# Kernel tuning notes

Hardware: AMD Instinct MI355X
Metric: run time of the kernel (lower is better)

The kernel has to match this reference:

```python
import jax, jax.numpy as jnp
import numpy as np
from jax import lax

N_HEAD, D_IN, D_HID, D_OUT = 8, 64, 64, 64
SEQ = 32768
STD = 1.0 / np.sqrt(D_HID * N_HEAD)


def _unif(key, shape):
    return jax.random.uniform(key, shape, jnp.float32, -STD, STD)


def setup_inputs() -> dict:
    key = jax.random.key(0)
    ks = jax.random.split(key, 12)
    D = N_HEAD * D_IN
    return {
        "inputs": jax.random.normal(ks[0], (SEQ, D), jnp.float32),
        "W_in": _unif(ks[1], (D, D)),
        "b_in": _unif(ks[2], (D,)),
        "W_gates": _unif(ks[3], (D_IN, 3 * D_HID)),
        "b_gates": _unif(ks[4], (3 * D_HID,)),
        "W_og": _unif(ks[5], (D_IN, D_HID)),
        "b_og": _unif(ks[6], (D_HID,)),
        "W_c": _unif(ks[7], (D_HID, D_OUT)),
        "b_c": _unif(ks[8], (D_OUT,)),
        "W_out": _unif(ks[9], (N_HEAD * D_OUT, N_HEAD * D_OUT)),
        "b_out": _unif(ks[10], (N_HEAD * D_OUT,)),
    }


def reference(inputs, W_in, b_in, W_gates, b_gates, W_og, b_og, W_c, b_c, W_out, b_out):
    S = inputs.shape[0]
    # input mixing across heads, then flatten: (S, H*d_in) -> (S*H, d_in)
    x = (inputs @ W_in + b_in).reshape(S * N_HEAD, D_IN)
    # FirstModule: fused gate projection
    g = x @ W_gates + b_gates  # (S*H, 3*d_hid)
    fg = jax.nn.sigmoid(g[:, :D_HID])
    ig = jax.nn.sigmoid(g[:, D_HID:2 * D_HID])
    h = jnp.tanh(g[:, 2 * D_HID:])
    hr = ig * h
    # linear recurrence c_t = fg_t * c_{t-1} + hr_t, c_0 = 0, via associative scan
    def comb(e1, e2):
        a1, b1 = e1
        a2, b2 = e2
        return (a1 * a2, b1 * a2 + b2)
    _, c = lax.associative_scan(comb, (fg, hr))  # (S*H, d_hid)
    # SecondModule: output gate and projection
    og = jax.nn.sigmoid(x @ W_og + b_og)
    o = (og * c) @ W_c + b_c  # (S*H, d_out)
    o = o.reshape(S, N_HEAD * D_OUT)
    return o @ W_out + b_out
```

## Files before the change

### kernel.cpp

```cpp
#include <hip/hip_runtime.h>


typedef unsigned short ushort;
typedef __bf16 bf16x8 __attribute__((ext_vector_type(8)));
typedef float f32x4 __attribute__((ext_vector_type(4)));

#define CROWS 64
#define NCH  4096
#define NSUP 64

#define GLOAD16(gp, lp) __builtin_amdgcn_global_load_lds( \
    (const __attribute__((address_space(1))) void*)(gp),  \
    (__attribute__((address_space(3))) void*)(lp), 16, 0, 0)

__device__ inline float b2f(ushort u) {
    return __builtin_bit_cast(float, (unsigned)u << 16);
}
__device__ inline ushort f2b(float f) {
    unsigned x = __builtin_bit_cast(unsigned, f);
    x += 0x7FFFu + ((x >> 16) & 1u);
    return (ushort)(x >> 16);
}
__device__ inline float sigm(float v) { return __builtin_amdgcn_rcpf(1.0f + __expf(-v)); }
__device__ inline float tanh_fast(float v) {
    return 2.0f * __builtin_amdgcn_rcpf(1.0f + __expf(-2.0f * v)) - 1.0f;
}
__device__ inline f32x4 MFMA(bf16x8 a, bf16x8 b, f32x4 c) {
    return __builtin_amdgcn_mfma_f32_16x16x32_bf16(a, b, c, 0, 0, 0);
}

__global__ void transpose512(const float* __restrict__ src, ushort* __restrict__ dst) {
    __shared__ float tile[32][33];
    const int tx = threadIdx.x & 31, ty = threadIdx.x >> 5;
    const int x0 = blockIdx.x * 32, y0 = blockIdx.y * 32;
    #pragma unroll
    for (int dy = 0; dy < 32; dy += 8)
        tile[ty + dy][tx] = src[(size_t)(y0 + ty + dy) * 512 + x0 + tx];
    __syncthreads();
    #pragma unroll
    for (int dy = 0; dy < 32; dy += 8)
        dst[(size_t)(x0 + ty + dy) * 512 + y0 + tx] = f2b(tile[tx][ty + dy]);
}

__global__ void prep_small(const float* __restrict__ W_gates, const float* __restrict__ W_og,
                           const float* __restrict__ W_c,
                           const float* __restrict__ b_gates, const float* __restrict__ b_og,
                           ushort* __restrict__ W2T, ushort* __restrict__ WcT, float* __restrict__ b2) {
    const int idx = blockIdx.x * 256 + threadIdx.x;
    if (idx < 16384) {
        const int n = idx >> 6, k = idx & 63;
        float v;
        if      (n < 64)  v = W_gates[k * 192 + 64 + n];
        else if (n < 128) v = W_gates[k * 192 + 128 + (n - 64)];
        else if (n < 192) v = W_gates[k * 192 + (n - 128)];
        else              v = W_og[k * 64 + (n - 192)];
        W2T[idx] = f2b(v);
    } else if (idx < 16384 + 4096) {
        const int i = idx - 16384;
        const int n = i >> 6, k = i & 63;
        WcT[i] = f2b(W_c[(k << 6) + n]);
    } else if (idx < 16384 + 4096 + 256) {
        const int i = idx - 20480;
        float v;
        if      (i < 64)  v = b_gates[64 + i];
        else if (i < 128) v = b_gates[128 + (i - 64)];
        else if (i < 192) v = b_gates[i - 128];
        else              v = b_og[i - 192];
        b2[i] = v;
    }
}

__global__ __launch_bounds__(256)
void cvt_f32_bf16(const float* __restrict__ src, ushort* __restrict__ dst) {
    const long i = ((long)blockIdx.x * 256 + threadIdx.x) * 8;
    const float4 v0 = *(const float4*)(src + i);
    const float4 v1 = *(const float4*)(src + i + 4);
    *(ushort4*)(dst + i)     = make_ushort4(f2b(v0.x), f2b(v0.y), f2b(v0.z), f2b(v0.w));
    *(ushort4*)(dst + i + 4) = make_ushort4(f2b(v1.x), f2b(v1.y), f2b(v1.z), f2b(v1.w));
}

template <int BM, int BN, int WAVES_M, int WAVES_N, int A32, int C32>
__global__ __launch_bounds__(256)
void gemm_bt(const void* __restrict__ Av, const ushort* __restrict__ Bt,
             const float* __restrict__ bias, void* __restrict__ Cv,
             int M, int N, int K) {
    constexpr int WM = BM / WAVES_M, WN = BN / WAVES_N;
    constexpr int MT = WM / 16, NT = WN / 16;
    __shared__ __align__(16) ushort sA[BM * 32];
    __shared__ __align__(16) ushort sB[BN * 32];

    const int t = threadIdx.x, w = t >> 6, lane = t & 63;
    const int wm = (w / WAVES_N) * WM, wn = (w % WAVES_N) * WN;
    const long bm = (long)blockIdx.x * BM, bn = (long)blockIdx.y * BN;

    f32x4 acc[MT][NT] = {};

    for (int k0 = 0; k0 < K; k0 += 32) {
        if (A32) {
            const float* A = (const float*)Av;
            #pragma unroll
            for (int is = 0; is < BM / 32; ++is) {
                const int row = is * 32 + (t >> 3);
                const int cd = (t & 7) >> 1, half = t & 1;
                const float4 v = *(const float4*)(A + (bm + row) * (long)K + k0 + (t & 7) * 4);
                *(ushort4*)&sA[row * 32 + ((cd ^ (row & 3)) * 8) + half * 4] =
                    make_ushort4(f2b(v.x), f2b(v.y), f2b(v.z), f2b(v.w));
            }
        } else {
            const ushort* A = (const ushort*)Av;
            #pragma unroll
            for (int is = 0; is < BM / 64; ++is) {
                const int row = t >> 2, kc = t & 3;
                GLOAD16(A + (bm + is * 64 + row) * (long)K + k0 + ((kc ^ (row & 3)) * 8),
                        (char*)sA + is * 4096 + w * 1024);
            }
        }
        #pragma unroll
        for (int is = 0; is < BN / 64; ++is) {
            const int row = t >> 2, kc = t & 3;
            GLOAD16(Bt + (bn + is * 64 + row) * (long)K + k0 + ((kc ^ (row & 3)) * 8),
                    (char*)sB + is * 4096 + w * 1024);
        }
        __syncthreads();

        bf16x8 af[MT], bfr[NT];
        #pragma unroll
        for (int i = 0; i < MT; ++i) {
            const int row = wm + i * 16 + (lane & 15), c = lane >> 4;
            af[i] = *(const bf16x8*)&sA[row * 32 + ((c ^ (row & 3)) * 8)];
        }
        #pragma unroll
        for (int j = 0; j < NT; ++j) {
            const int rb = wn + j * 16 + (lane & 15), c = lane >> 4;
            bfr[j] = *(const bf16x8*)&sB[rb * 32 + ((c ^ (rb & 3)) * 8)];
        }
        #pragma unroll
        for (int i = 0; i < MT; ++i)
            #pragma unroll
            for (int j = 0; j < NT; ++j)
                acc[i][j] = MFMA(af[i], bfr[j], acc[i][j]);
        __syncthreads();
    }

    #pragma unroll
    for (int i = 0; i < MT; ++i)
        #pragma unroll
        for (int j = 0; j < NT; ++j) {
            const long col = bn + wn + j * 16 + (lane & 15);
            const float bv = bias[col];
            #pragma unroll
            for (int r = 0; r < 4; ++r) {
                const long row = bm + wm + i * 16 + ((lane >> 4) << 2) + r;
                const float v = acc[i][j][r] + bv;
                if (C32) ((float*)Cv)[row * (long)N + col] = v;
                else     ((ushort*)Cv)[row * (long)N + col] = f2b(v);
            }
        }
}

__global__ __launch_bounds__(256, 4)
void gates_store(const ushort* __restrict__ X, const ushort* __restrict__ W2T,
                 const float* __restrict__ b2,
                 unsigned* __restrict__ FGHR, ushort* __restrict__ OGg,
                 float* __restrict__ Agg, float* __restrict__ Bgg) {
    __shared__ __align__(16) char smem[29696];
    ushort* sFG = (ushort*)smem;
    ushort* sHR = (ushort*)(smem + 9216);
    ushort* sOG = (ushort*)(smem + 18432);
    float*  spa = (float*)(smem + 27648);
    float*  spb = (float*)(smem + 28672);

    const int t = threadIdx.x, w = t >> 6, lane = t & 63;
    const int blk = blockIdx.x;
    const long row0 = (long)blk * CROWS;

    const int wm = (w >> 1) * 32;
    const int grpB = w & 1;
    const int colbase = grpB * 128;
    const int lr = lane & 15, lc = lane >> 4;

    bf16x8 af[2][2];
    #pragma unroll
    for (int kk = 0; kk < 2; ++kk)
        #pragma unroll
        for (int i = 0; i < 2; ++i)
            af[kk][i] = *(const bf16x8*)(X + (row0 + wm + i * 16 + lr) * 64 + kk * 32 + lc * 8);

    f32x4 acc[2][8] = {};
    #pragma unroll
    for (int kk = 0; kk < 2; ++kk)
        #pragma unroll
        for (int j = 0; j < 8; ++j) {
            const bf16x8 bf = *(const bf16x8*)(W2T + (colbase + j * 16 + lr) * 64 + kk * 32 + lc * 8);
            acc[0][j] = MFMA(af[kk][0], bf, acc[0][j]);
            acc[1][j] = MFMA(af[kk][1], bf, acc[1][j]);
        }

    if (!grpB) {
        #pragma unroll
        for (int jj = 0; jj < 4; ++jj) {
            const int ch = jj * 16 + lr;
            const float bi = b2[ch], bh = b2[64 + ch];
            #pragma unroll
            for (int i = 0; i < 2; ++i)
                #pragma unroll
                for (int r = 0; r < 4; ++r) {
                    const int row = wm + i * 16 + (lc << 2) + r;
                    const float gi = acc[i][jj][r] + bi;
                    const float gh = acc[i][jj + 4][r] + bh;
                    sHR[row * 72 + ch] = f2b(sigm(gi) * tanh_fast(gh));
                }
        }
    } else {
        #pragma unroll
        for (int jj = 0; jj < 4; ++jj) {
            const int ch = jj * 16 + lr;
            const float bfg = b2[128 + ch], bog = b2[192 + ch];
            #pragma unroll
            for (int i = 0; i < 2; ++i)
                #pragma unroll
                for (int r = 0; r < 4; ++r) {
                    const int row = wm + i * 16 + (lc << 2) + r;
                    sFG[row * 72 + ch] = f2b(sigm(acc[i][jj][r] + bfg));
                    sOG[row * 72 + ch] = f2b(sigm(acc[i][jj + 4][r] + bog));
                }
        }
    }
    __syncthreads();

    {
        const int ch = lane;
        float a = 1.0f, b = 0.0f;
        #pragma unroll
        for (int r = 0; r < 16; ++r) {
            const int row = (w << 4) + r;
            const ushort ufg = sFG[row * 72 + ch];
            const ushort uhr = sHR[row * 72 + ch];
            FGHR[(row0 + row) * 64 + ch] = (unsigned)ufg | ((unsigned)uhr << 16);
            OGg[(row0 + row) * 64 + ch] = sOG[row * 72 + ch];
            const float fg = b2f(ufg), hr = b2f(uhr);
            a *= fg;
            b = fmaf(b, fg, hr);
        }
        spa[(w << 6) + ch] = a;
        spb[(w << 6) + ch] = b;
    }
    __syncthreads();

    if (t < 64) {
        float a = spa[t], b = spb[t];
        #pragma unroll
        for (int k = 1; k < 4; ++k) {
            const float a2 = spa[(k << 6) + t];
            const float bb = spb[(k << 6) + t];
            a *= a2;
            b = fmaf(b, a2, bb);
        }
        Agg[blk * 64 + t] = a;
        Bgg[blk * 64 + t] = b;
    }
}

__global__ __launch_bounds__(256, 4)
void scan_apply(const unsigned* __restrict__ FGHR, const ushort* __restrict__ OGg,
                const float* __restrict__ Agg, const float* __restrict__ Bgg,
                const float* __restrict__ PreS,
                const ushort* __restrict__ WcT, const float* __restrict__ b_c,
                ushort* __restrict__ O) {
    __shared__ __align__(16) char smem[10240];
    ushort* sP  = (ushort*)smem;
    float*  spa = (float*)(smem + 8192);
    float*  spb = (float*)(smem + 9216);

    const int t = threadIdx.x, w = t >> 6, lane = t & 63;
    const int blk = blockIdx.x;
    const long row0 = (long)blk * CROWS;
    const int ch = lane;

    unsigned fh[16];
    {
        float a = 1.0f, b = 0.0f;
        #pragma unroll
        for (int r = 0; r < 16; ++r) {
            fh[r] = FGHR[(row0 + (w << 4) + r) * 64 + ch];
            const float fg = b2f((ushort)fh[r]);
            const float hr = b2f((ushort)(fh[r] >> 16));
            a *= fg;
            b = fmaf(b, fg, hr);
        }
        spa[(w << 6) + ch] = a;
        spb[(w << 6) + ch] = b;
    }
    __syncthreads();

    float c = fmaf(PreS[(blk >> 6) * 64 + ch], Agg[blk * 64 + ch], Bgg[blk * 64 + ch]);
    for (int k = 0; k < w; ++k)
        c = fmaf(c, spa[(k << 6) + ch], spb[(k << 6) + ch]);

    const int cch = ch >> 3, half = ch & 7;
    #pragma unroll
    for (int r = 0; r < 16; ++r) {
        const int row = (w << 4) + r;
        const float fg = b2f((ushort)fh[r]);
        const float hr = b2f((ushort)(fh[r] >> 16));
        c = fmaf(c, fg, hr);
        const float og = b2f(OGg[(row0 + row) * 64 + ch]);
        sP[row * 64 + ((cch ^ (row & 7)) * 8) + half] = f2b(og * c);
    }
    __syncthreads();

    const int wm = (w >> 1) * 32;
    const int wn2 = (w & 1) * 32;
    const int lr = lane & 15, lc = lane >> 4;
    f32x4 acc2[2][2] = {};
    #pragma unroll
    for (int kk = 0; kk < 2; ++kk) {
        bf16x8 pa[2], wb[2];
        #pragma unroll
        for (int i = 0; i < 2; ++i) {
            const int row = wm + i * 16 + lr, cidx = kk * 4 + lc;
            pa[i] = *(const bf16x8*)&sP[row * 64 + ((cidx ^ (row & 7)) * 8)];
        }
        #pragma unroll
        for (int j = 0; j < 2; ++j)
            wb[j] = *(const bf16x8*)(WcT + (wn2 + j * 16 + lr) * 64 + kk * 32 + lc * 8);
        #pragma unroll
        for (int i = 0; i < 2; ++i)
            #pragma unroll
            for (int j = 0; j < 2; ++j)
                acc2[i][j] = MFMA(pa[i], wb[j], acc2[i][j]);
    }
    #pragma unroll
    for (int i = 0; i < 2; ++i)
        #pragma unroll
        for (int j = 0; j < 2; ++j) {
            const int col = wn2 + j * 16 + lr;
            const float bv = b_c[col];
            #pragma unroll
            for (int r = 0; r < 4; ++r) {
                const int row = wm + i * 16 + (lc << 2) + r;
                O[(row0 + row) * 64 + col] = f2b(acc2[i][j][r] + bv);
            }
        }
}

template <int APPLY>
__global__ __launch_bounds__(256, 4)
void gates_scan(const ushort* __restrict__ X, const ushort* __restrict__ W2T,
                const float* __restrict__ b2, const ushort* __restrict__ WcT,
                const float* __restrict__ b_c,
                float* __restrict__ Agg, float* __restrict__ Bgg,
                const float* __restrict__ PreS, ushort* __restrict__ O) {
    __shared__ __align__(16) char smem[APPLY ? 35840 : 18432];
    ushort* sFG = (ushort*)smem;
    ushort* sHR = (ushort*)(smem + 9216);
    ushort* sOG = (ushort*)(smem + 18432);
    ushort* sP  = (ushort*)(smem + 27648);

    const int t = threadIdx.x, w = t >> 6, lane = t & 63;
    const int blk = blockIdx.x;
    const long row0 = (long)blk * CROWS;

    const int wm = (w >> 1) * 32;
    const int grpB = w & 1;
    const int colbase = grpB * 128;
    const int lr = lane & 15, lc = lane >> 4;

    bf16x8 af[2][2];
    #pragma unroll
    for (int kk = 0; kk < 2; ++kk)
        #pragma unroll
        for (int i = 0; i < 2; ++i)
            af[kk][i] = *(const bf16x8*)(X + (row0 + wm + i * 16 + lr) * 64 + kk * 32 + lc * 8);

    f32x4 acc[2][8] = {};
    #pragma unroll
    for (int kk = 0; kk < 2; ++kk)
        #pragma unroll
        for (int j = 0; j < 8; ++j) {
            const bf16x8 bf = *(const bf16x8*)(W2T + (colbase + j * 16 + lr) * 64 + kk * 32 + lc * 8);
            acc[0][j] = MFMA(af[kk][0], bf, acc[0][j]);
            acc[1][j] = MFMA(af[kk][1], bf, acc[1][j]);
        }

    if (!grpB) {
        #pragma unroll
        for (int jj = 0; jj < 4; ++jj) {
            const int ch = jj * 16 + lr;
            const float bi = b2[ch], bh = b2[64 + ch];
            #pragma unroll
            for (int i = 0; i < 2; ++i)
                #pragma unroll
                for (int r = 0; r < 4; ++r) {
                    const int row = wm + i * 16 + (lc << 2) + r;
                    const float gi = acc[i][jj][r] + bi;
                    const float gh = acc[i][jj + 4][r] + bh;
                    sHR[row * 72 + ch] = f2b(sigm(gi) * tanh_fast(gh));
                }
        }
    } else {
        #pragma unroll
        for (int jj = 0; jj < 4; ++jj) {
            const int ch = jj * 16 + lr;
            const float bfg = b2[128 + ch], bog = b2[192 + ch];
            #pragma unroll
            for (int i = 0; i < 2; ++i)
                #pragma unroll
                for (int r = 0; r < 4; ++r) {
                    const int row = wm + i * 16 + (lc << 2) + r;
                    sFG[row * 72 + ch] = f2b(sigm(acc[i][jj][r] + bfg));
                    if (APPLY) sOG[row * 72 + ch] = f2b(sigm(acc[i][jj + 4][r] + bog));
                }
        }
    }
    __syncthreads();

    if (!APPLY) {
        if (t < 64) {
            float a = 1.0f, b = 0.0f;
            #pragma unroll 8
            for (int r = 0; r < CROWS; ++r) {
                const float fg = b2f(sFG[r * 72 + t]);
                const float hr = b2f(sHR[r * 72 + t]);
                a *= fg;
                b = fmaf(b, fg, hr);
            }
            Agg[blk * 64 + t] = a;
            Bgg[blk * 64 + t] = b;
        }
        return;
    }

    if (t < 64) {
        float c = fmaf(PreS[(blk >> 6) * 64 + t], Agg[blk * 64 + t], Bgg[blk * 64 + t]);
        const int cch = t >> 3, half = t & 7;
        #pragma unroll 8
        for (int r = 0; r < CROWS; ++r) {
            const float fg = b2f(sFG[r * 72 + t]);
            const float hr = b2f(sHR[r * 72 + t]);
            c = fmaf(c, fg, hr);
            sP[r * 64 + ((cch ^ (r & 7)) * 8) + half] = f2b(b2f(sOG[r * 72 + t]) * c);
        }
    }
    __syncthreads();

    const int wn2 = grpB * 32;
    f32x4 acc2[2][2] = {};
    #pragma unroll
    for (int kk = 0; kk < 2; ++kk) {
        bf16x8 pa[2], wb[2];
        #pragma unroll
        for (int i = 0; i < 2; ++i) {
            const int row = wm + i * 16 + lr, c = kk * 4 + lc;
            pa[i] = *(const bf16x8*)&sP[row * 64 + ((c ^ (row & 7)) * 8)];
        }
        #pragma unroll
        for (int j = 0; j < 2; ++j)
            wb[j] = *(const bf16x8*)(WcT + (wn2 + j * 16 + lr) * 64 + kk * 32 + lc * 8);
        #pragma unroll
        for (int i = 0; i < 2; ++i)
            #pragma unroll
            for (int j = 0; j < 2; ++j)
                acc2[i][j] = MFMA(pa[i], wb[j], acc2[i][j]);
    }
    #pragma unroll
    for (int i = 0; i < 2; ++i)
        #pragma unroll
        for (int j = 0; j < 2; ++j) {
            const int col = wn2 + j * 16 + lr;
            const float bv = b_c[col];
            #pragma unroll
            for (int r = 0; r < 4; ++r) {
                const int row = wm + i * 16 + (lc << 2) + r;
                O[(row0 + row) * 64 + col] = f2b(acc2[i][j][r] + bv);
            }
        }
}

__global__ void scan_super(float* __restrict__ Agg, float* __restrict__ Bgg,
                           float* __restrict__ SA, float* __restrict__ SB) {
    const int s = blockIdx.x, ch = threadIdx.x;
    float a = 1.0f, b = 0.0f;
    #pragma unroll 8
    for (int j = 0; j < 64; ++j) {
        const int idx = (s * 64 + j) * 64 + ch;
        const float a2 = Agg[idx], bb = Bgg[idx];
        Agg[idx] = a;
        Bgg[idx] = b;
        a *= a2;
        b = fmaf(b, a2, bb);
    }
    SA[s * 64 + ch] = a;
    SB[s * 64 + ch] = b;
}

__global__ void scan_top(const float* __restrict__ SA, const float* __restrict__ SB,
                         float* __restrict__ PreS) {
    const int ch = threadIdx.x;
    float c = 0.0f;
    #pragma unroll 8
    for (int s = 0; s < 64; ++s) {
        PreS[s * 64 + ch] = c;
        c = fmaf(c, SA[s * 64 + ch], SB[s * 64 + ch]);
    }
}

extern "C" void kernel_launch(void* const* d_in, const int* in_sizes, int n_in,
                              void* d_out, int out_size, void* d_ws, size_t ws_size,
                              hipStream_t stream) {
    const float* inputs  = (const float*)d_in[0];
    const float* W_in    = (const float*)d_in[1];
    const float* b_in    = (const float*)d_in[2];
    const float* W_gates = (const float*)d_in[3];
    const float* b_gates = (const float*)d_in[4];
    const float* W_og    = (const float*)d_in[5];
    const float* b_og    = (const float*)d_in[6];
    const float* W_c     = (const float*)d_in[7];
    const float* b_c     = (const float*)d_in[8];
    const float* W_out   = (const float*)d_in[9];
    const float* b_out   = (const float*)d_in[10];
    float* out = (float*)d_out;

    char* ws = (char*)d_ws;
    ushort* X     = (ushort*)(ws);
    ushort* WinT  = (ushort*)(ws + 33554432);
    ushort* WoutT = (ushort*)(ws + 34078720);
    ushort* W2T   = (ushort*)(ws + 34603008);
    ushort* WcT   = (ushort*)(ws + 34635776);
    float*  b2    = (float*)(ws + 34643968);
    float*  Agg   = (float*)(ws + 34644992);
    float*  Bgg   = (float*)(ws + 35693568);
    float*  SA    = (float*)(ws + 36742144);
    float*  SB    = (float*)(ws + 36758528);
    float*  PreS  = (float*)(ws + 36774912);
    ushort* Ibf   = (ushort*)(ws + 36791296);
    unsigned* FGHR = (unsigned*)(ws + 36791296);
    ushort* OGg   = (ushort*)d_out;
    ushort* O = X;

    const bool new_path = ws_size >= 103900160ull;
    const bool big_ws   = ws_size >= 70345728ull;

    transpose512<<<dim3(16, 16), 256, 0, stream>>>(W_in, WinT);
    transpose512<<<dim3(16, 16), 256, 0, stream>>>(W_out, WoutT);
    prep_small<<<81, 256, 0, stream>>>(W_gates, W_og, W_c, b_gates, b_og, W2T, WcT, b2);

    if (new_path) {
        cvt_f32_bf16<<<8192, 256, 0, stream>>>(inputs, Ibf);
        gemm_bt<128, 128, 2, 2, 0, 0><<<dim3(256, 4), 256, 0, stream>>>(
            Ibf, WinT, b_in, X, 32768, 512, 512);
        gates_store<<<NCH, 256, 0, stream>>>(X, W2T, b2, FGHR, OGg, Agg, Bgg);
        scan_super<<<NSUP, 64, 0, stream>>>(Agg, Bgg, SA, SB);
        scan_top<<<1, 64, 0, stream>>>(SA, SB, PreS);
        scan_apply<<<NCH, 256, 0, stream>>>(FGHR, OGg, Agg, Bgg, PreS, WcT, b_c, O);
    } else if (big_ws) {
        cvt_f32_bf16<<<8192, 256, 0, stream>>>(inputs, Ibf);
        gemm_bt<128, 128, 2, 2, 0, 0><<<dim3(256, 4), 256, 0, stream>>>(
            Ibf, WinT, b_in, X, 32768, 512, 512);
        gates_scan<0><<<NCH, 256, 0, stream>>>(X, W2T, b2, WcT, b_c, Agg, Bgg, PreS, O);
        scan_super<<<NSUP, 64, 0, stream>>>(Agg, Bgg, SA, SB);
        scan_top<<<1, 64, 0, stream>>>(SA, SB, PreS);
        gates_scan<1><<<NCH, 256, 0, stream>>>(X, W2T, b2, WcT, b_c, Agg, Bgg, PreS, O);
    } else {
        gemm_bt<128, 128, 2, 2, 1, 0><<<dim3(256, 4), 256, 0, stream>>>(
            inputs, WinT, b_in, X, 32768, 512, 512);
        gates_scan<0><<<NCH, 256, 0, stream>>>(X, W2T, b2, WcT, b_c, Agg, Bgg, PreS, O);
        scan_super<<<NSUP, 64, 0, stream>>>(Agg, Bgg, SA, SB);
        scan_top<<<1, 64, 0, stream>>>(SA, SB, PreS);
        gates_scan<1><<<NCH, 256, 0, stream>>>(X, W2T, b2, WcT, b_c, Agg, Bgg, PreS, O);
    }

    gemm_bt<128, 128, 2, 2, 0, 1><<<dim3(256, 4), 256, 0, stream>>>(
        O, WoutT, b_out, out, 32768, 512, 512);
}
```

Before: 288.6 us.

## Recompute output gate in scan_apply instead of storing it from gates_store

The output-gate projection and sigmoid move from gates_store into scan_apply, which reloads X and the og slice of W2T and recomputes og with MFMAs into shared memory. This removes a global write and a later read of the bf16 OG tensor, which is the same size as the per-head activation. In exchange, X is read a second time in scan_apply and a few more MFMAs are added there. gates_store uses less LDS and declares a higher launch_bounds occupancy target to fit more blocks per CU.

```diff
diff --git a/kernel.cpp b/kernel.cpp
--- a/kernel.cpp
+++ b/kernel.cpp
@@ -158,17 +158,16 @@
         }
 }
 
-__global__ __launch_bounds__(256, 4)
+__global__ __launch_bounds__(256, 6)
 void gates_store(const ushort* __restrict__ X, const ushort* __restrict__ W2T,
                  const float* __restrict__ b2,
-                 unsigned* __restrict__ FGHR, ushort* __restrict__ OGg,
+                 unsigned* __restrict__ FGHR,
                  float* __restrict__ Agg, float* __restrict__ Bgg) {
-    __shared__ __align__(16) char smem[29696];
+    __shared__ __align__(16) char smem[20480];
     ushort* sFG = (ushort*)smem;
     ushort* sHR = (ushort*)(smem + 9216);
-    ushort* sOG = (ushort*)(smem + 18432);
-    float*  spa = (float*)(smem + 27648);
-    float*  spb = (float*)(smem + 28672);
+    float*  spa = (float*)(smem + 18432);
+    float*  spb = (float*)(smem + 19456);
 
     const int t = threadIdx.x, w = t >> 6, lane = t & 63;
     const int blk = blockIdx.x;
@@ -176,7 +175,6 @@
 
     const int wm = (w >> 1) * 32;
     const int grpB = w & 1;
-    const int colbase = grpB * 128;
     const int lr = lane & 15, lc = lane >> 4;
 
     bf16x8 af[2][2];
@@ -187,14 +185,25 @@
             af[kk][i] = *(const bf16x8*)(X + (row0 + wm + i * 16 + lr) * 64 + kk * 32 + lc * 8);
 
     f32x4 acc[2][8] = {};
-    #pragma unroll
-    for (int kk = 0; kk < 2; ++kk)
-        #pragma unroll
-        for (int j = 0; j < 8; ++j) {
-            const bf16x8 bf = *(const bf16x8*)(W2T + (colbase + j * 16 + lr) * 64 + kk * 32 + lc * 8);
-            acc[0][j] = MFMA(af[kk][0], bf, acc[0][j]);
-            acc[1][j] = MFMA(af[kk][1], bf, acc[1][j]);
-        }
+    if (!grpB) {
+        #pragma unroll
+        for (int kk = 0; kk < 2; ++kk)
+            #pragma unroll
+            for (int j = 0; j < 8; ++j) {
+                const bf16x8 bf = *(const bf16x8*)(W2T + (j * 16 + lr) * 64 + kk * 32 + lc * 8);
+                acc[0][j] = MFMA(af[kk][0], bf, acc[0][j]);
+                acc[1][j] = MFMA(af[kk][1], bf, acc[1][j]);
+            }
+    } else {
+        #pragma unroll
+        for (int kk = 0; kk < 2; ++kk)
+            #pragma unroll
+            for (int j = 0; j < 4; ++j) {
+                const bf16x8 bf = *(const bf16x8*)(W2T + ((128 + j * 16 + lr)) * 64 + kk * 32 + lc * 8);
+                acc[0][j] = MFMA(af[kk][0], bf, acc[0][j]);
+                acc[1][j] = MFMA(af[kk][1], bf, acc[1][j]);
+            }
+    }
 
     if (!grpB) {
         #pragma unroll
@@ -215,14 +224,13 @@
         #pragma unroll
         for (int jj = 0; jj < 4; ++jj) {
             const int ch = jj * 16 + lr;
-            const float bfg = b2[128 + ch], bog = b2[192 + ch];
+            const float bfg = b2[128 + ch];
             #pragma unroll
             for (int i = 0; i < 2; ++i)
                 #pragma unroll
                 for (int r = 0; r < 4; ++r) {
                     const int row = wm + i * 16 + (lc << 2) + r;
                     sFG[row * 72 + ch] = f2b(sigm(acc[i][jj][r] + bfg));
-                    sOG[row * 72 + ch] = f2b(sigm(acc[i][jj + 4][r] + bog));
                 }
         }
     }
@@ -237,7 +245,6 @@
             const ushort ufg = sFG[row * 72 + ch];
             const ushort uhr = sHR[row * 72 + ch];
             FGHR[(row0 + row) * 64 + ch] = (unsigned)ufg | ((unsigned)uhr << 16);
-            OGg[(row0 + row) * 64 + ch] = sOG[row * 72 + ch];
             const float fg = b2f(ufg), hr = b2f(uhr);
             a *= fg;
             b = fmaf(b, fg, hr);
@@ -262,20 +269,36 @@
 }
 
 __global__ __launch_bounds__(256, 4)
-void scan_apply(const unsigned* __restrict__ FGHR, const ushort* __restrict__ OGg,
+void scan_apply(const unsigned* __restrict__ FGHR, const ushort* __restrict__ X,
+                const ushort* __restrict__ W2T, const float* __restrict__ b2,
                 const float* __restrict__ Agg, const float* __restrict__ Bgg,
                 const float* __restrict__ PreS,
                 const ushort* __restrict__ WcT, const float* __restrict__ b_c,
                 ushort* __restrict__ O) {
-    __shared__ __align__(16) char smem[10240];
+    __shared__ __align__(16) char smem[19456];
     ushort* sP  = (ushort*)smem;
-    float*  spa = (float*)(smem + 8192);
-    float*  spb = (float*)(smem + 9216);
+    ushort* sOG = (ushort*)(smem + 8192);
+    float*  spa = (float*)(smem + 17408);
+    float*  spb = (float*)(smem + 18432);
 
     const int t = threadIdx.x, w = t >> 6, lane = t & 63;
     const int blk = blockIdx.x;
     const long row0 = (long)blk * CROWS;
     const int ch = lane;
+    const int lr = lane & 15, lc = lane >> 4;
+    const int wm = (w >> 1) * 32;
+    const int wno = (w & 1) * 32;
+
+    bf16x8 af[2][2], wb[2][2];
+    #pragma unroll
+    for (int kk = 0; kk < 2; ++kk) {
+        #pragma unroll
+        for (int i = 0; i < 2; ++i)
+            af[kk][i] = *(const bf16x8*)(X + (row0 + wm + i * 16 + lr) * 64 + kk * 32 + lc * 8);
+        #pragma unroll
+        for (int j = 0; j < 2; ++j)
+            wb[kk][j] = *(const bf16x8*)(W2T + (192 + wno + j * 16 + lr) * 64 + kk * 32 + lc * 8);
+    }
 
     unsigned fh[16];
     {
@@ -291,6 +314,29 @@
         spa[(w << 6) + ch] = a;
         spb[(w << 6) + ch] = b;
     }
+
+    {
+        f32x4 aog[2][2] = {};
+        #pragma unroll
+        for (int kk = 0; kk < 2; ++kk)
+            #pragma unroll
+            for (int i = 0; i < 2; ++i)
+                #pragma unroll
+                for (int j = 0; j < 2; ++j)
+                    aog[i][j] = MFMA(af[kk][i], wb[kk][j], aog[i][j]);
+        #pragma unroll
+        for (int i = 0; i < 2; ++i)
+            #pragma unroll
+            for (int j = 0; j < 2; ++j) {
+                const int col = wno + j * 16 + lr;
+                const float bog = b2[192 + col];
+                #pragma unroll
+                for (int r = 0; r < 4; ++r) {
+                    const int row = wm + i * 16 + (lc << 2) + r;
+                    sOG[row * 72 + col] = f2b(sigm(aog[i][j][r] + bog));
+                }
+            }
+    }
     __syncthreads();
 
     float c = fmaf(PreS[(blk >> 6) * 64 + ch], Agg[blk * 64 + ch], Bgg[blk * 64 + ch]);
@@ -304,18 +350,15 @@
         const float fg = b2f((ushort)fh[r]);
         const float hr = b2f((ushort)(fh[r] >> 16));
         c = fmaf(c, fg, hr);
-        const float og = b2f(OGg[(row0 + row) * 64 + ch]);
+        const float og = b2f(sOG[row * 72 + ch]);
         sP[row * 64 + ((cch ^ (row & 7)) * 8) + half] = f2b(og * c);
     }
     __syncthreads();
 
-    const int wm = (w >> 1) * 32;
-    const int wn2 = (w & 1) * 32;
-    const int lr = lane & 15, lc = lane >> 4;
     f32x4 acc2[2][2] = {};
     #pragma unroll
     for (int kk = 0; kk < 2; ++kk) {
-        bf16x8 pa[2], wb[2];
+        bf16x8 pa[2], wc[2];
         #pragma unroll
         for (int i = 0; i < 2; ++i) {
             const int row = wm + i * 16 + lr, cidx = kk * 4 + lc;
@@ -323,18 +366,18 @@
         }
         #pragma unroll
         for (int j = 0; j < 2; ++j)
-            wb[j] = *(const bf16x8*)(WcT + (wn2 + j * 16 + lr) * 64 + kk * 32 + lc * 8);
+            wc[j] = *(const bf16x8*)(WcT + (wno + j * 16 + lr) * 64 + kk * 32 + lc * 8);
         #pragma unroll
         for (int i = 0; i < 2; ++i)
             #pragma unroll
             for (int j = 0; j < 2; ++j)
-                acc2[i][j] = MFMA(pa[i], wb[j], acc2[i][j]);
+                acc2[i][j] = MFMA(pa[i], wc[j], acc2[i][j]);
     }
     #pragma unroll
     for (int i = 0; i < 2; ++i)
         #pragma unroll
         for (int j = 0; j < 2; ++j) {
-            const int col = wn2 + j * 16 + lr;
+            const int col = wno + j * 16 + lr;
             const float bv = b_c[col];
             #pragma unroll
             for (int r = 0; r < 4; ++r) {
@@ -448,7 +491,7 @@
     f32x4 acc2[2][2] = {};
     #pragma unroll
     for (int kk = 0; kk < 2; ++kk) {
-        bf16x8 pa[2], wb[2];
+        bf16x8 pa[2], wbx[2];
         #pragma unroll
         for (int i = 0; i < 2; ++i) {
             const int row = wm + i * 16 + lr, c = kk * 4 + lc;
@@ -456,12 +499,12 @@
         }
         #pragma unroll
         for (int j = 0; j < 2; ++j)
-            wb[j] = *(const bf16x8*)(WcT + (wn2 + j * 16 + lr) * 64 + kk * 32 + lc * 8);
+            wbx[j] = *(const bf16x8*)(WcT + (wn2 + j * 16 + lr) * 64 + kk * 32 + lc * 8);
         #pragma unroll
         for (int i = 0; i < 2; ++i)
             #pragma unroll
             for (int j = 0; j < 2; ++j)
-                acc2[i][j] = MFMA(pa[i], wb[j], acc2[i][j]);
+                acc2[i][j] = MFMA(pa[i], wbx[j], acc2[i][j]);
     }
     #pragma unroll
     for (int i = 0; i < 2; ++i)
@@ -535,7 +578,6 @@
     float*  PreS  = (float*)(ws + 36774912);
     ushort* Ibf   = (ushort*)(ws + 36791296);
     unsigned* FGHR = (unsigned*)(ws + 36791296);
-    ushort* OGg   = (ushort*)d_out;
     ushort* O = X;
 
     const bool new_path = ws_size >= 103900160ull;
@@ -549,10 +591,10 @@
         cvt_f32_bf16<<<8192, 256, 0, stream>>>(inputs, Ibf);
         gemm_bt<128, 128, 2, 2, 0, 0><<<dim3(256, 4), 256, 0, stream>>>(
             Ibf, WinT, b_in, X, 32768, 512, 512);
-        gates_store<<<NCH, 256, 0, stream>>>(X, W2T, b2, FGHR, OGg, Agg, Bgg);
+        gates_store<<<NCH, 256, 0, stream>>>(X, W2T, b2, FGHR, Agg, Bgg);
         scan_super<<<NSUP, 64, 0, stream>>>(Agg, Bgg, SA, SB);
         scan_top<<<1, 64, 0, stream>>>(SA, SB, PreS);
-        scan_apply<<<NCH, 256, 0, stream>>>(FGHR, OGg, Agg, Bgg, PreS, WcT, b_c, O);
+        scan_apply<<<NCH, 256, 0, stream>>>(FGHR, X, W2T, b2, Agg, Bgg, PreS, WcT, b_c, O);
     } else if (big_ws) {
         cvt_f32_bf16<<<8192, 256, 0, stream>>>(inputs, Ibf);
         gemm_bt<128, 128, 2, 2, 0, 0><<<dim3(256, 4), 256, 0, stream>>>(
```

Result: slower. 318.8 us (+10.5%).

## Fuse gate, scan and output projection via decoupled look-back scan

Applied to the files above, without the earlier changes.

Replaces the gates_store / scan_super / scan_top / scan_apply chain with one gates_fused kernel. It uses a single-pass decoupled look-back scan: each chunk publishes its aggregate and inclusive prefix through 64-bit atomic flags, which cvt_f32_bf16 initialises. This removes the FGHR/OGg intermediate round trip through global memory and three kernel launches. It also merges sigmoid/tanh pairs so they share one reciprocal. The cost is serial spin-waiting between consecutive blocks and a dependence on blocks being scheduled roughly in order, plus slightly more LDS per block.

```diff
diff --git a/kernel.cpp b/kernel.cpp
--- a/kernel.cpp
+++ b/kernel.cpp
@@ -8,6 +8,7 @@
 #define CROWS 64
 #define NCH  4096
 #define NSUP 64
+#define EMPTY64 0xFFFFFFFFFFFFFFFFull
 
 #define GLOAD16(gp, lp) __builtin_amdgcn_global_load_lds( \
     (const __attribute__((address_space(1))) void*)(gp),  \
@@ -71,7 +72,10 @@
 }
 
 __global__ __launch_bounds__(256)
-void cvt_f32_bf16(const float* __restrict__ src, ushort* __restrict__ dst) {
+void cvt_f32_bf16(const float* __restrict__ src, ushort* __restrict__ dst,
+                  unsigned long long* __restrict__ P1, unsigned long long* __restrict__ P2) {
+    const int j = blockIdx.x * 256 + threadIdx.x;
+    if (P1 != nullptr && j < NCH * 64) { P1[j] = EMPTY64; P2[j] = EMPTY64; }
     const long i = ((long)blockIdx.x * 256 + threadIdx.x) * 8;
     const float4 v0 = *(const float4*)(src + i);
     const float4 v1 = *(const float4*)(src + i + 4);
@@ -159,16 +163,20 @@
 }
 
 __global__ __launch_bounds__(256, 4)
-void gates_store(const ushort* __restrict__ X, const ushort* __restrict__ W2T,
-                 const float* __restrict__ b2,
-                 unsigned* __restrict__ FGHR, ushort* __restrict__ OGg,
-                 float* __restrict__ Agg, float* __restrict__ Bgg) {
-    __shared__ __align__(16) char smem[29696];
+void gates_fused(const ushort* __restrict__ X, const ushort* __restrict__ W2T,
+                 const float* __restrict__ b2, const ushort* __restrict__ WcT,
+                 const float* __restrict__ b_c,
+                 unsigned long long* __restrict__ Ppart,
+                 unsigned long long* __restrict__ Pincl,
+                 ushort* __restrict__ O) {
+    __shared__ __align__(16) char smem[38400];
     ushort* sFG = (ushort*)smem;
     ushort* sHR = (ushort*)(smem + 9216);
     ushort* sOG = (ushort*)(smem + 18432);
-    float*  spa = (float*)(smem + 27648);
-    float*  spb = (float*)(smem + 28672);
+    ushort* sP  = (ushort*)(smem + 27648);
+    float*  spa = (float*)(smem + 35840);
+    float*  spb = (float*)(smem + 36864);
+    float*  sCin= (float*)(smem + 37888);
 
     const int t = threadIdx.x, w = t >> 6, lane = t & 63;
     const int blk = blockIdx.x;
@@ -208,7 +216,10 @@
                     const int row = wm + i * 16 + (lc << 2) + r;
                     const float gi = acc[i][jj][r] + bi;
                     const float gh = acc[i][jj + 4][r] + bh;
-                    sHR[row * 72 + ch] = f2b(sigm(gi) * tanh_fast(gh));
+                    const float A = __expf(-gi);
+                    const float B = __expf(-2.0f * gh);
+                    const float hr = (1.0f - B) * __builtin_amdgcn_rcpf((1.0f + A) * (1.0f + B));
+                    sHR[row * 72 + ch] = f2b(hr);
                 }
         }
     } else {
@@ -221,29 +232,28 @@
                 #pragma unroll
                 for (int r = 0; r < 4; ++r) {
                     const int row = wm + i * 16 + (lc << 2) + r;
-                    sFG[row * 72 + ch] = f2b(sigm(acc[i][jj][r] + bfg));
-                    sOG[row * 72 + ch] = f2b(sigm(acc[i][jj + 4][r] + bog));
+                    const float C = __expf(-(acc[i][jj][r] + bfg));
+                    const float D = __expf(-(acc[i][jj + 4][r] + bog));
+                    const float R = __builtin_amdgcn_rcpf((1.0f + C) * (1.0f + D));
+                    sFG[row * 72 + ch] = f2b((1.0f + D) * R);
+                    sOG[row * 72 + ch] = f2b((1.0f + C) * R);
                 }
         }
     }
     __syncthreads();
 
     {
-        const int ch = lane;
         float a = 1.0f, b = 0.0f;
         #pragma unroll
         for (int r = 0; r < 16; ++r) {
             const int row = (w << 4) + r;
-            const ushort ufg = sFG[row * 72 + ch];
-            const ushort uhr = sHR[row * 72 + ch];
-            FGHR[(row0 + row) * 64 + ch] = (unsigned)ufg | ((unsigned)uhr << 16);
-            OGg[(row0 + row) * 64 + ch] = sOG[row * 72 + ch];
-            const float fg = b2f(ufg), hr = b2f(uhr);
+            const float fg = b2f(sFG[row * 72 + lane]);
+            const float hr = b2f(sHR[row * 72 + lane]);
             a *= fg;
             b = fmaf(b, fg, hr);
         }
-        spa[(w << 6) + ch] = a;
-        spb[(w << 6) + ch] = b;
+        spa[(w << 6) + lane] = a;
+        spb[(w << 6) + lane] = b;
     }
     __syncthreads();
 
@@ -256,79 +266,77 @@
             a *= a2;
             b = fmaf(b, a2, bb);
         }
-        Agg[blk * 64 + t] = a;
-        Bgg[blk * 64 + t] = b;
-    }
-}
-
-__global__ __launch_bounds__(256, 4)
-void scan_apply(const unsigned* __restrict__ FGHR, const ushort* __restrict__ OGg,
-                const float* __restrict__ Agg, const float* __restrict__ Bgg,
-                const float* __restrict__ PreS,
-                const ushort* __restrict__ WcT, const float* __restrict__ b_c,
-                ushort* __restrict__ O) {
-    __shared__ __align__(16) char smem[10240];
-    ushort* sP  = (ushort*)smem;
-    float*  spa = (float*)(smem + 8192);
-    float*  spb = (float*)(smem + 9216);
-
-    const int t = threadIdx.x, w = t >> 6, lane = t & 63;
-    const int blk = blockIdx.x;
-    const long row0 = (long)blk * CROWS;
-    const int ch = lane;
-
-    unsigned fh[16];
+        const long me = (long)blk * 64 + t;
+        __hip_atomic_store(&Ppart[me],
+            ((unsigned long long)__builtin_bit_cast(unsigned, b) << 32) |
+             (unsigned long long)__builtin_bit_cast(unsigned, a),
+            __ATOMIC_RELAXED, __HIP_MEMORY_SCOPE_AGENT);
+
+        float run_a = 1.0f, run_b = 0.0f, c_in = 0.0f;
+        int p = blk - 1;
+        bool done = (blk == 0);
+        while (!done) {
+            const unsigned long long vi = __hip_atomic_load(&Pincl[(long)p * 64 + t],
+                __ATOMIC_RELAXED, __HIP_MEMORY_SCOPE_AGENT);
+            if (vi != EMPTY64) {
+                c_in = fmaf(__builtin_bit_cast(float, (unsigned)(vi >> 32)), run_a, run_b);
+                done = true;
+            } else {
+                const unsigned long long pp = __hip_atomic_load(&Ppart[(long)p * 64 + t],
+                    __ATOMIC_RELAXED, __HIP_MEMORY_SCOPE_AGENT);
+                if (pp != EMPTY64) {
+                    const float ap = __builtin_bit_cast(float, (unsigned)pp);
+                    const float bp = __builtin_bit_cast(float, (unsigned)(pp >> 32));
+                    run_b = fmaf(bp, run_a, run_b);
+                    run_a *= ap;
+                    if (--p < 0) { c_in = run_b; done = true; }
+                } else {
+                    __builtin_amdgcn_s_sleep(1);
+                }
+            }
+        }
+        const float v = fmaf(c_in, a, b);
+        __hip_atomic_store(&Pincl[me],
+            ((unsigned long long)__builtin_bit_cast(unsigned, v) << 32) | 1ull,
+            __ATOMIC_RELAXED, __HIP_MEMORY_SCOPE_AGENT);
+        sCin[t] = c_in;
+    }
+    __syncthreads();
+
     {
-        float a = 1.0f, b = 0.0f;
+        float c = sCin[lane];
+        for (int k = 0; k < w; ++k)
+            c = fmaf(c, spa[(k << 6) + lane], spb[(k << 6) + lane]);
+        const int cch = lane >> 3, half = lane & 7;
         #pragma unroll
         for (int r = 0; r < 16; ++r) {
-            fh[r] = FGHR[(row0 + (w << 4) + r) * 64 + ch];
-            const float fg = b2f((ushort)fh[r]);
-            const float hr = b2f((ushort)(fh[r] >> 16));
-            a *= fg;
-            b = fmaf(b, fg, hr);
-        }
-        spa[(w << 6) + ch] = a;
-        spb[(w << 6) + ch] = b;
-    }
-    __syncthreads();
-
-    float c = fmaf(PreS[(blk >> 6) * 64 + ch], Agg[blk * 64 + ch], Bgg[blk * 64 + ch]);
-    for (int k = 0; k < w; ++k)
-        c = fmaf(c, spa[(k << 6) + ch], spb[(k << 6) + ch]);
-
-    const int cch = ch >> 3, half = ch & 7;
-    #pragma unroll
-    for (int r = 0; r < 16; ++r) {
-        const int row = (w << 4) + r;
-        const float fg = b2f((ushort)fh[r]);
-        const float hr = b2f((ushort)(fh[r] >> 16));
-        c = fmaf(c, fg, hr);
-        const float og = b2f(OGg[(row0 + row) * 64 + ch]);
-        sP[row * 64 + ((cch ^ (row & 7)) * 8) + half] = f2b(og * c);
-    }
-    __syncthreads();
-
-    const int wm = (w >> 1) * 32;
-    const int wn2 = (w & 1) * 32;
-    const int lr = lane & 15, lc = lane >> 4;
+            const int row = (w << 4) + r;
+            const float fg = b2f(sFG[row * 72 + lane]);
+            const float hr = b2f(sHR[row * 72 + lane]);
+            c = fmaf(c, fg, hr);
+            sP[row * 64 + ((cch ^ (row & 7)) * 8) + half] = f2b(b2f(sOG[row * 72 + lane]) * c);
+        }
+    }
+    __syncthreads();
+
+    const int wn2 = grpB * 32;
     f32x4 acc2[2][2] = {};
     #pragma unroll
     for (int kk = 0; kk < 2; ++kk) {
-        bf16x8 pa[2], wb[2];
+        bf16x8 pa[2], wbx[2];
         #pragma unroll
         for (int i = 0; i < 2; ++i) {
-            const int row = wm + i * 16 + lr, cidx = kk * 4 + lc;
-            pa[i] = *(const bf16x8*)&sP[row * 64 + ((cidx ^ (row & 7)) * 8)];
+            const int row = wm + i * 16 + lr, c = kk * 4 + lc;
+            pa[i] = *(const bf16x8*)&sP[row * 64 + ((c ^ (row & 7)) * 8)];
         }
         #pragma unroll
         for (int j = 0; j < 2; ++j)
-            wb[j] = *(const bf16x8*)(WcT + (wn2 + j * 16 + lr) * 64 + kk * 32 + lc * 8);
+            wbx[j] = *(const bf16x8*)(WcT + (wn2 + j * 16 + lr) * 64 + kk * 32 + lc * 8);
         #pragma unroll
         for (int i = 0; i < 2; ++i)
             #pragma unroll
             for (int j = 0; j < 2; ++j)
-                acc2[i][j] = MFMA(pa[i], wb[j], acc2[i][j]);
+                acc2[i][j] = MFMA(pa[i], wbx[j], acc2[i][j]);
     }
     #pragma unroll
     for (int i = 0; i < 2; ++i)
@@ -448,7 +456,7 @@
     f32x4 acc2[2][2] = {};
     #pragma unroll
     for (int kk = 0; kk < 2; ++kk) {
-        bf16x8 pa[2], wb[2];
+        bf16x8 pa[2], wbx[2];
         #pragma unroll
         for (int i = 0; i < 2; ++i) {
             const int row = wm + i * 16 + lr, c = kk * 4 + lc;
@@ -456,12 +464,12 @@
         }
         #pragma unroll
         for (int j = 0; j < 2; ++j)
-            wb[j] = *(const bf16x8*)(WcT + (wn2 + j * 16 + lr) * 64 + kk * 32 + lc * 8);
+            wbx[j] = *(const bf16x8*)(WcT + (wn2 + j * 16 + lr) * 64 + kk * 32 + lc * 8);
         #pragma unroll
         for (int i = 0; i < 2; ++i)
             #pragma unroll
             for (int j = 0; j < 2; ++j)
-                acc2[i][j] = MFMA(pa[i], wb[j], acc2[i][j]);
+                acc2[i][j] = MFMA(pa[i], wbx[j], acc2[i][j]);
     }
     #pragma unroll
     for (int i = 0; i < 2; ++i)
@@ -534,27 +542,24 @@
     float*  SB    = (float*)(ws + 36758528);
     float*  PreS  = (float*)(ws + 36774912);
     ushort* Ibf   = (ushort*)(ws + 36791296);
-    unsigned* FGHR = (unsigned*)(ws + 36791296);
-    ushort* OGg   = (ushort*)d_out;
+    unsigned long long* Ppart = (unsigned long long*)(ws + 70345728);
+    unsigned long long* Pincl = (unsigned long long*)(ws + 72442880);
     ushort* O = X;
 
-    const bool new_path = ws_size >= 103900160ull;
-    const bool big_ws   = ws_size >= 70345728ull;
+    const bool lb_ws  = ws_size >= 74539008ull;
+    const bool big_ws = ws_size >= 70345728ull;
 
     transpose512<<<dim3(16, 16), 256, 0, stream>>>(W_in, WinT);
     transpose512<<<dim3(16, 16), 256, 0, stream>>>(W_out, WoutT);
     prep_small<<<81, 256, 0, stream>>>(W_gates, W_og, W_c, b_gates, b_og, W2T, WcT, b2);
 
-    if (new_path) {
-        cvt_f32_bf16<<<8192, 256, 0, stream>>>(inputs, Ibf);
+    if (lb_ws) {
+        cvt_f32_bf16<<<8192, 256, 0, stream>>>(inputs, Ibf, Ppart, Pincl);
         gemm_bt<128, 128, 2, 2, 0, 0><<<dim3(256, 4), 256, 0, stream>>>(
             Ibf, WinT, b_in, X, 32768, 512, 512);
-        gates_store<<<NCH, 256, 0, stream>>>(X, W2T, b2, FGHR, OGg, Agg, Bgg);
-        scan_super<<<NSUP, 64, 0, stream>>>(Agg, Bgg, SA, SB);
-        scan_top<<<1, 64, 0, stream>>>(SA, SB, PreS);
-        scan_apply<<<NCH, 256, 0, stream>>>(FGHR, OGg, Agg, Bgg, PreS, WcT, b_c, O);
+        gates_fused<<<NCH, 256, 0, stream>>>(X, W2T, b2, WcT, b_c, Ppart, Pincl, O);
     } else if (big_ws) {
-        cvt_f32_bf16<<<8192, 256, 0, stream>>>(inputs, Ibf);
+        cvt_f32_bf16<<<8192, 256, 0, stream>>>(inputs, Ibf, nullptr, nullptr);
         gemm_bt<128, 128, 2, 2, 0, 0><<<dim3(256, 4), 256, 0, stream>>>(
             Ibf, WinT, b_in, X, 32768, 512, 512);
         gates_scan<0><<<NCH, 256, 0, stream>>>(X, W2T, b2, WcT, b_c, Agg, Bgg, PreS, O);
```

Measured after the change: 310.6 us. 7.6% more time.
